# Kernel optimization log

Measured on AMD Instinct MI355X. Metric: run time of the kernel, lower is better.

The kernel has to match this reference:

```python
import jax, jax.numpy as jnp
import numpy as np

N_HEAD = 16
D_HEAD = 64
D_MODEL = 1024
N_ROLL = 3
SCALE = 1.0 / (D_HEAD ** 0.5)
EPS = 1e-5


def mul_roll_repeat(x, n_roll):
    # concat of x * roll(x, i) over i=1..n_roll along last dim
    return jnp.concatenate([x * jnp.roll(x, i, axis=-1) for i in range(1, n_roll + 1)], axis=-1)


def dpfp(x):
    # DPFP feature map: [relu(x), relu(-x)] then roll-multiply-repeat
    x2 = jnp.concatenate([jax.nn.relu(x), jax.nn.relu(-x)], axis=-1)
    return mul_roll_repeat(x2, N_ROLL)


def layer_norm(x, gamma, beta):
    mu = jnp.mean(x, axis=-1, keepdims=True)
    var = jnp.var(x, axis=-1, keepdims=True)
    return (x - mu) * jax.lax.rsqrt(var + 1e-5) * gamma + beta


def setup_inputs() -> dict:
    key = jax.random.key(0)
    ks = jax.random.split(key, 4)
    S, B = 2048, 2
    h = jax.random.normal(ks[0], (S, B, D_MODEL), dtype=jnp.float32)
    Wq = jax.random.normal(ks[1], (D_MODEL, N_HEAD * D_HEAD), dtype=jnp.float32) * 0.02
    Wkv = jax.random.normal(ks[2], (D_MODEL, 2 * N_HEAD * D_HEAD), dtype=jnp.float32) * 0.02
    Wo = jax.random.normal(ks[3], (N_HEAD * D_HEAD, D_MODEL), dtype=jnp.float32) * 0.02
    ln_gamma = jnp.ones((D_MODEL,), dtype=jnp.float32)
    ln_beta = jnp.zeros((D_MODEL,), dtype=jnp.float32)
    return {"h": h, "Wq": Wq, "Wkv": Wkv, "Wo": Wo, "ln_gamma": ln_gamma, "ln_beta": ln_beta}


def reference(h, Wq, Wkv, Wo, ln_gamma, ln_beta):
    # h: [S, B, D_MODEL]; mems=None, attn_mask=None, post-LN, eval (no dropout)
    S, B, _ = h.shape
    q = (h @ Wq).reshape(S, B, N_HEAD, D_HEAD)
    kv = h @ Wkv
    k, v = jnp.split(kv, 2, axis=-1)
    k = k.reshape(S, B, N_HEAD, D_HEAD)
    v = v.reshape(S, B, N_HEAD, D_HEAD)

    pq = dpfp(q)  # [S, B, N, F], F = 2*D_HEAD*N_ROLL = 384
    pk = dpfp(k)

    # Linear-attention form: identical math to the original quadratic
    # einsum('ibnd,jbnd->ijbn') * scale, summed over j for the denominator,
    # since there is no mask and dropatt=0. Avoids the O(S^2) score tensor.
    kv_agg = jnp.einsum('jbnf,jbnd->bnfd', pk, v)          # [B, N, F, D]
    z = pk.sum(axis=0)                                      # [B, N, F]
    num = jnp.einsum('ibnf,bnfd->ibnd', pq, kv_agg) * SCALE  # [S, B, N, D]
    den = jnp.einsum('ibnf,bnf->ibn', pq, z) * SCALE + EPS   # [S, B, N]
    attn_vec = (num / den[..., None]).reshape(S, B, N_HEAD * D_HEAD)

    attn_out = attn_vec @ Wo
    return layer_norm(h + attn_out, ln_gamma, ln_beta)
```

## Files before the change

### kernel.cpp

```cpp
#include <hip/hip_runtime.h>
#include <math.h>

#define NH 16
#define DM 1024
#define FEAT 384
#define SB 4096
#define SEQ 2048

static constexpr float SCALE = 0.125f;
static constexpr float EPS = 1e-5f;

typedef __attribute__((ext_vector_type(8))) _Float16 half8;
typedef __attribute__((ext_vector_type(4))) _Float16 half4;
typedef __attribute__((ext_vector_type(4))) float f32x4;

#define AS1 __attribute__((address_space(1)))
#define AS3 __attribute__((address_space(3)))

#define IDX(r, o) ((((r) << 6)) + ((((o) ^ ((r) & 7))) << 3))

__global__ __launch_bounds__(256) void prep_kernel(const float* __restrict__ h,
                                                   const float* __restrict__ Wq,
                                                   const float* __restrict__ Wkv,
                                                   const float* __restrict__ Wo,
                                                   _Float16* __restrict__ h_h,
                                                   _Float16* __restrict__ WqkvT,
                                                   _Float16* __restrict__ WoT) {
    __shared__ _Float16 tile[32][33];
    int bid = blockIdx.x, t = threadIdx.x;
    if (bid < 4096) {
        int i = bid * 256 + t;
        const float4 v = ((const float4*)h)[i];
        half4 o = {(_Float16)v.x, (_Float16)v.y, (_Float16)v.z, (_Float16)v.w};
        ((half4*)h_h)[i] = o;
        return;
    }
    const float* src;
    _Float16* dst;
    int N, col0, n0, k0;
    if (bid < 7168) {
        int b2 = bid - 4096;
        n0 = (b2 % 96) * 32; k0 = (b2 / 96) * 32;
        if (n0 < 1024) { src = Wq; N = 1024; col0 = n0; }
        else           { src = Wkv; N = 2048; col0 = n0 - 1024; }
        dst = WqkvT;
    } else {
        int b3 = bid - 7168;
        n0 = (b3 & 31) * 32; k0 = (b3 >> 5) * 32;
        src = Wo; N = 1024; col0 = n0; dst = WoT;
    }
    int tx = t & 31, ty = t >> 5;
    #pragma unroll
    for (int i = 0; i < 4; ++i)
        tile[ty + i * 8][tx] = (_Float16)src[(size_t)(k0 + ty + i * 8) * N + col0 + tx];
    __syncthreads();
    #pragma unroll
    for (int i = 0; i < 4; ++i)
        dst[(size_t)(n0 + ty + i * 8) * 1024 + k0 + tx] = tile[tx][ty + i * 8];
}

template <int MH>
__device__ __forceinline__ void mfma_all(f32x4 (&acc)[8][3], half8 (&a)[4][2],
                                         half8 (&bv)[3][2]) {
    #pragma unroll
    for (int mf = 0; mf < 4; ++mf)
        #pragma unroll
        for (int nf = 0; nf < 3; ++nf)
            #pragma unroll
            for (int ks = 0; ks < 2; ++ks)
                acc[MH * 4 + mf][nf] = __builtin_amdgcn_mfma_f32_16x16x32_f16(
                    a[mf][ks], bv[nf][ks], acc[MH * 4 + mf][nf], 0, 0, 0);
}

__global__ __launch_bounds__(512) void gemm_f16_8ph(const _Float16* __restrict__ A,
                                                    const _Float16* __restrict__ BT,
                                                    _Float16* __restrict__ C,
                                                    int M, int N, int K) {
    __shared__ _Float16 smem[57344];
    const int t = threadIdx.x;
    const int w = t >> 6, l = t & 63;
    const int wr = w >> 2, wc = w & 3;
    const int NT = K >> 6;
    const int NU = K >> 4;

    int nwg = gridDim.x;
    int cpx = nwg >> 3;
    int bid = blockIdx.x;
    int swz = (bid & 7) * cpx + (bid >> 3);
    int ntile = N / 192;
    int row0 = (swz / ntile) << 8;
    int col0 = (swz % ntile) * 192;

    f32x4 acc[8][3];
    #pragma unroll
    for (int m = 0; m < 8; ++m)
        #pragma unroll
        for (int n = 0; n < 3; ++n)
            acc[m][n] = (f32x4){0.f, 0.f, 0.f, 0.f};

    const int lr = l >> 3;
    const int lc8 = ((l & 7) ^ lr) * 8;

    auto STAGE = [&](int s) {
        if (s >= NU) return;
        int tau = s >> 2, u = s & 3;
        int kk = tau << 6;
        int bufo = (tau & 1) * 28672;
        if (u == 0) {
            #pragma unroll
            for (int i = 0; i < 2; ++i) {
                int chunk = w * 2 + i;
                const _Float16* src = BT + (size_t)(col0 + chunk * 8 + lr) * K + kk + lc8;
                __builtin_amdgcn_global_load_lds((const AS1 void*)src,
                    (AS3 void*)(smem + bufo + 16384 + chunk * 512), 16, 0, 0);
            }
        } else if (u == 1) {
            const _Float16* src = BT + (size_t)(col0 + 128 + w * 8 + lr) * K + kk + lc8;
            __builtin_amdgcn_global_load_lds((const AS1 void*)src,
                (AS3 void*)(smem + bufo + 24576 + w * 512), 16, 0, 0);
        } else {
            int rbase = (u == 3) ? 128 : 0;
            int lbase = (u == 3) ? 8192 : 0;
            #pragma unroll
            for (int i = 0; i < 2; ++i) {
                int chunk = w * 2 + i;
                const _Float16* src = A + (size_t)(row0 + rbase + chunk * 8 + lr) * K + kk + lc8;
                __builtin_amdgcn_global_load_lds((const AS1 void*)src,
                    (AS3 void*)(smem + bufo + lbase + chunk * 512), 16, 0, 0);
            }
        }
    };

    half8 a[4][2], bv[3][2];
    auto LDA = [&](int mh, int bufo) {
        #pragma unroll
        for (int mf = 0; mf < 4; ++mf) {
            int r = wr * 128 + (mh * 4 + mf) * 16 + (l & 15);
            #pragma unroll
            for (int ks = 0; ks < 2; ++ks) {
                int c16 = (ks * 4 + (l >> 4)) ^ (r & 7);
                a[mf][ks] = *(const half8*)&smem[bufo + r * 64 + c16 * 8];
            }
        }
    };
    auto LDB = [&](int bufo) {
        #pragma unroll
        for (int nf = 0; nf < 3; ++nf) {
            int r = wc * 48 + nf * 16 + (l & 15);
            #pragma unroll
            for (int ks = 0; ks < 2; ++ks) {
                int c16 = (ks * 4 + (l >> 4)) ^ (r & 7);
                bv[nf][ks] = *(const half8*)&smem[bufo + 16384 + r * 64 + c16 * 8];
            }
        }
    };

    STAGE(0); STAGE(1);
    STAGE(2); STAGE(3);
    STAGE(4); STAGE(5);
    asm volatile("s_waitcnt vmcnt(3)" ::: "memory");
    __builtin_amdgcn_s_barrier();

    #pragma unroll 1
    for (int ti = 0; ti < NT; ++ti) {
        const int bufo = (ti & 1) * 28672;
        const int sb = (ti + 1) << 2;
        LDA(0, bufo); LDB(bufo);
        STAGE(sb + 2); STAGE(sb + 3);
        __builtin_amdgcn_sched_barrier(0);
        __builtin_amdgcn_s_barrier();
        asm volatile("s_waitcnt lgkmcnt(0)" ::: "memory");
        __builtin_amdgcn_sched_barrier(0);
        __builtin_amdgcn_s_setprio(1);
        mfma_all<0>(acc, a, bv);
        __builtin_amdgcn_s_setprio(0);
        __builtin_amdgcn_sched_barrier(0);
        __builtin_amdgcn_s_barrier();
        LDA(1, bufo);
        STAGE(sb + 4); STAGE(sb + 5);
        __builtin_amdgcn_sched_barrier(0);
        __builtin_amdgcn_s_barrier();
        asm volatile("s_waitcnt lgkmcnt(0)" ::: "memory");
        __builtin_amdgcn_sched_barrier(0);
        __builtin_amdgcn_s_setprio(1);
        mfma_all<1>(acc, a, bv);
        __builtin_amdgcn_s_setprio(0);
        __builtin_amdgcn_sched_barrier(0);
        if (ti < NT - 2) asm volatile("s_waitcnt vmcnt(3)" ::: "memory");
        else             asm volatile("s_waitcnt vmcnt(0)" ::: "memory");
        __builtin_amdgcn_s_barrier();
    }

    int ocol = l & 15, orow4 = (l >> 4) * 4;
    #pragma unroll
    for (int mf = 0; mf < 8; ++mf)
        #pragma unroll
        for (int nf = 0; nf < 3; ++nf) {
            size_t base = (size_t)(row0 + wr * 128 + mf * 16 + orow4) * N
                        + col0 + wc * 48 + nf * 16 + ocol;
            #pragma unroll
            for (int j = 0; j < 4; ++j)
                C[base + (size_t)j * N] = (_Float16)acc[mf][nf][j];
        }
}

__global__ __launch_bounds__(256) void gemm_f16(const _Float16* __restrict__ A,
                                                const _Float16* __restrict__ BT,
                                                _Float16* __restrict__ C,
                                                int M, int N, int K) {
    __shared__ _Float16 Asb[128 * 32];
    __shared__ _Float16 Bsb[128 * 32];
    int t = threadIdx.x;
    int w = t >> 6, l = t & 63;
    int wr = w >> 1, wc = w & 1;
    int row0 = blockIdx.y * 128, col0 = blockIdx.x * 128;

    f32x4 acc[4][4];
    #pragma unroll
    for (int m = 0; m < 4; ++m)
        #pragma unroll
        for (int n = 0; n < 4; ++n)
            acc[m][n] = (f32x4){0.f, 0.f, 0.f, 0.f};

    int srow = l >> 2;
    int scol = (l & 3) * 8;

    for (int k0 = 0; k0 < K; k0 += 32) {
        #pragma unroll
        for (int i = 0; i < 2; ++i) {
            int chunk = w * 2 + i;
            const _Float16* asrc =
                A + (size_t)(row0 + chunk * 16 + srow) * K + k0 + scol;
            __builtin_amdgcn_global_load_lds((const AS1 void*)asrc,
                                             (AS3 void*)(Asb + chunk * 512), 16, 0, 0);
            const _Float16* bsrc =
                BT + (size_t)(col0 + chunk * 16 + srow) * K + k0 + scol;
            __builtin_amdgcn_global_load_lds((const AS1 void*)bsrc,
                                             (AS3 void*)(Bsb + chunk * 512), 16, 0, 0);
        }
        __syncthreads();
        int rsel = l & 15, csel = (l >> 4) * 8;
        half8 a[4], b[4];
        #pragma unroll
        for (int m = 0; m < 4; ++m)
            a[m] = *(const half8*)&Asb[(wr * 64 + m * 16 + rsel) * 32 + csel];
        #pragma unroll
        for (int n = 0; n < 4; ++n)
            b[n] = *(const half8*)&Bsb[(wc * 64 + n * 16 + rsel) * 32 + csel];
        #pragma unroll
        for (int m = 0; m < 4; ++m)
            #pragma unroll
            for (int n = 0; n < 4; ++n)
                acc[m][n] = __builtin_amdgcn_mfma_f32_16x16x32_f16(a[m], b[n], acc[m][n], 0, 0, 0);
        __syncthreads();
    }

    int ocol = l & 15, orow = (l >> 4) * 4;
    #pragma unroll
    for (int m = 0; m < 4; ++m)
        #pragma unroll
        for (int n = 0; n < 4; ++n) {
            size_t base = (size_t)(row0 + wr * 64 + m * 16 + orow) * N
                        + col0 + wc * 64 + n * 16 + ocol;
            #pragma unroll
            for (int j = 0; j < 4; ++j)
                C[base + (size_t)j * N] = (_Float16)acc[m][n][j];
        }
}

__global__ __launch_bounds__(512) void kvagg_fused(const _Float16* __restrict__ qkv,
                                                   float* __restrict__ kvp,
                                                   float* __restrict__ zp) {
    __shared__ _Float16 x2s[128 * 64];
    __shared__ _Float16 vTs[64 * 64];
    __shared__ _Float16 pkTs[384 * 64];
    const int t = threadIdx.x;
    const int w = t >> 6, l = t & 63;
    const int bn = blockIdx.x;
    const int jseg = blockIdx.y;
    const int b = bn >> 4, nh = bn & 15;

    f32x4 acc[4][3];
    #pragma unroll
    for (int mf = 0; mf < 4; ++mf)
        #pragma unroll
        for (int nf = 0; nf < 3; ++nf)
            acc[mf][nf] = (f32x4){0.f, 0.f, 0.f, 0.f};
    float zacc[3] = {0.f, 0.f, 0.f};

    const int sc = t & 63;
    const int so = t >> 6;

    #pragma unroll 1
    for (int ch = 0; ch < 4; ++ch) {
        int j0 = jseg * 256 + ch * 64;
        _Float16 kx[8], vx[8];
        #pragma unroll
        for (int e = 0; e < 8; ++e) {
            size_t rb = (size_t)((j0 + so * 8 + e) * 2 + b) * 3072 + nh * 64 + sc;
            kx[e] = qkv[rb + 1024];
            vx[e] = qkv[rb + 2048];
        }
        half8 xlo, xhi, vv;
        #pragma unroll
        for (int e = 0; e < 8; ++e) {
            float kf = (float)kx[e];
            xlo[e] = (_Float16)fmaxf(kf, 0.f);
            xhi[e] = (_Float16)fmaxf(-kf, 0.f);
            vv[e] = vx[e];
        }
        if (ch) __syncthreads();
        *(half8*)&x2s[IDX(sc, so)] = xlo;
        *(half8*)&x2s[IDX(sc + 64, so)] = xhi;
        *(half8*)&vTs[IDX(sc, so)] = vv;
        __syncthreads();
        {
            const int o = t & 7;
            const int fb = t >> 3;
            #pragma unroll
            for (int it = 0; it < 6; ++it) {
                int f = it * 64 + fb;
                int fm = f & 127;
                int r = (f >> 7) + 1;
                int fm2 = (fm - r) & 127;
                half8 pa = *(const half8*)&x2s[IDX(fm, o)];
                half8 pb = *(const half8*)&x2s[IDX(fm2, o)];
                *(half8*)&pkTs[IDX(f, o)] = pa * pb;
            }
        }
        __syncthreads();
        #pragma unroll
        for (int ks = 0; ks < 2; ++ks) {
            half8 a[4], bq[3];
            int oo = ks * 4 + (l >> 4);
            #pragma unroll
            for (int mf = 0; mf < 4; ++mf) {
                int dr = mf * 16 + (l & 15);
                a[mf] = *(const half8*)&vTs[IDX(dr, oo)];
            }
            #pragma unroll
            for (int nf = 0; nf < 3; ++nf) {
                int fr = w * 48 + nf * 16 + (l & 15);
                bq[nf] = *(const half8*)&pkTs[IDX(fr, oo)];
                #pragma unroll
                for (int e = 0; e < 8; ++e) zacc[nf] += (float)bq[nf][e];
            }
            #pragma unroll
            for (int mf = 0; mf < 4; ++mf)
                #pragma unroll
                for (int nf = 0; nf < 3; ++nf)
                    acc[mf][nf] = __builtin_amdgcn_mfma_f32_16x16x32_f16(
                        a[mf], bq[nf], acc[mf][nf], 0, 0, 0);
        }
    }

    #pragma unroll
    for (int nf = 0; nf < 3; ++nf) {
        float v = zacc[nf];
        v += __shfl_xor(v, 16, 64);
        v += __shfl_xor(v, 32, 64);
        if (l < 16)
            zp[(size_t)(jseg * 32 + bn) * FEAT + w * 48 + nf * 16 + l] = v;
    }
    float* outp = kvp + (size_t)(jseg * 32 + bn) * 64 * FEAT;
    int orow = (l >> 4) * 4, ocol = l & 15;
    #pragma unroll
    for (int mf = 0; mf < 4; ++mf)
        #pragma unroll
        for (int nf = 0; nf < 3; ++nf) {
            int fcol = w * 48 + nf * 16 + ocol;
            #pragma unroll
            for (int j = 0; j < 4; ++j)
                outp[(size_t)(mf * 16 + orow + j) * FEAT + fcol] = acc[mf][nf][j];
        }
}

__global__ __launch_bounds__(256) void reduceA(const float* __restrict__ kvp,
                                               const float* __restrict__ zp,
                                               _Float16* __restrict__ kvaggT,
                                               float* __restrict__ z) {
    const int NKV = 32 * 64 * FEAT;
    int idx = blockIdx.x * 256 + threadIdx.x;
    if (idx < NKV) {
        float s = 0.f;
        #pragma unroll
        for (int c = 0; c < 8; ++c) s += kvp[(size_t)c * NKV + idx];
        kvaggT[idx] = (_Float16)s;
    } else if (idx < NKV + 32 * FEAT) {
        int e = idx - NKV;
        float s = 0.f;
        #pragma unroll
        for (int c = 0; c < 8; ++c) s += zp[c * 32 * FEAT + e];
        z[e] = s;
    }
}

template <int F0>
__device__ __forceinline__ void pq_half(const float (&qr)[64], _Float16* prow) {
    #pragma unroll
    for (int g8 = 0; g8 < 24; ++g8) {
        half8 o;
        #pragma unroll
        for (int e = 0; e < 8; ++e) {
            const int f = F0 + g8 * 8 + e;
            const int fm = f & 127;
            const int r = (f >> 7) + 1;
            const int fm2 = (fm - r) & 127;
            float a = (fm < 64) ? fmaxf(qr[fm], 0.f) : fmaxf(-qr[fm - 64], 0.f);
            float bb = (fm2 < 64) ? fmaxf(qr[fm2], 0.f) : fmaxf(-qr[fm2 - 64], 0.f);
            o[e] = (_Float16)(a * bb);
        }
        *(half8*)&prow[F0 + g8 * 8] = o;
    }
}

#define PQ_STR 392
__global__ __launch_bounds__(256) void attn_fused(const _Float16* __restrict__ qkv,
                                                  const _Float16* __restrict__ kvaggT,
                                                  const float* __restrict__ z,
                                                  _Float16* __restrict__ av) {
    __shared__ _Float16 pq_lds[128 * PQ_STR];
    __shared__ _Float16 B_lds[64 * PQ_STR];
    __shared__ float z_lds[FEAT];
    __shared__ float den_lds[128];
    int t = threadIdx.x;
    int w = t >> 6, l = t & 63;
    int iblk = blockIdx.x;
    int bn = blockIdx.y;
    int b = bn >> 4, nh = bn & 15;

    {
        const _Float16* Bg = kvaggT + (size_t)bn * 64 * FEAT;
        #pragma unroll
        for (int s = 0; s < 12; ++s) {
            int idx8 = t + 256 * s;
            half8 vv = *(const half8*)&Bg[idx8 * 8];
            int row = idx8 / 48, col8 = idx8 - row * 48;
            *(half8*)&B_lds[row * PQ_STR + col8 * 8] = vv;
        }
    }
    for (int e = t; e < FEAT; e += 256) z_lds[e] = z[(size_t)bn * FEAT + e];

    {
        int il = t & 127;
        int ig = iblk * 128 + il;
        const _Float16* qrow = qkv + ((size_t)ig * 2 + b) * 3072 + nh * 64;
        float qr[64];
        #pragma unroll
        for (int e2 = 0; e2 < 8; ++e2) {
            half8 vv = *(const half8*)&qrow[e2 * 8];
            #pragma unroll
            for (int e = 0; e < 8; ++e) qr[e2 * 8 + e] = (float)vv[e];
        }
        _Float16* prow = &pq_lds[il * PQ_STR];
        if (t < 128) pq_half<0>(qr, prow);
        else         pq_half<192>(qr, prow);
    }
    __syncthreads();

    f32x4 acc[2][4];
    #pragma unroll
    for (int m = 0; m < 2; ++m)
        #pragma unroll
        for (int n = 0; n < 4; ++n)
            acc[m][n] = (f32x4){0.f, 0.f, 0.f, 0.f};
    float denacc[2] = {0.f, 0.f};
    int rsel = l & 15, csel = (l >> 4) * 8;

    #pragma unroll
    for (int k0 = 0; k0 < FEAT; k0 += 32) {
        half8 a[2], bfr[4];
        #pragma unroll
        for (int m = 0; m < 2; ++m)
            a[m] = *(const half8*)&pq_lds[(w * 32 + m * 16 + rsel) * PQ_STR + k0 + csel];
        #pragma unroll
        for (int n = 0; n < 4; ++n)
            bfr[n] = *(const half8*)&B_lds[(n * 16 + rsel) * PQ_STR + k0 + csel];
        #pragma unroll
        for (int m = 0; m < 2; ++m)
            #pragma unroll
            for (int e = 0; e < 8; ++e)
                denacc[m] += (float)a[m][e] * z_lds[k0 + csel + e];
        #pragma unroll
        for (int m = 0; m < 2; ++m)
            #pragma unroll
            for (int n = 0; n < 4; ++n)
                acc[m][n] = __builtin_amdgcn_mfma_f32_16x16x32_f16(a[m], bfr[n], acc[m][n], 0, 0, 0);
    }

    #pragma unroll
    for (int m = 0; m < 2; ++m) {
        float v = denacc[m];
        v += __shfl_xor(v, 16, 64);
        v += __shfl_xor(v, 32, 64);
        if (l < 16) den_lds[w * 32 + m * 16 + l] = v;
    }
    __syncthreads();

    int orow = (l >> 4) * 4, ocol = l & 15;
    #pragma unroll
    for (int m = 0; m < 2; ++m)
        #pragma unroll
        for (int n = 0; n < 4; ++n)
            #pragma unroll
            for (int j = 0; j < 4; ++j) {
                int row = w * 32 + m * 16 + orow + j;
                float den = den_lds[row] * SCALE + EPS;
                float val = acc[m][n][j] * SCALE / den;
                int i = iblk * 128 + row;
                av[((size_t)i * 2 + b) * 1024 + nh * 64 + n * 16 + ocol] = (_Float16)val;
            }
}

__global__ __launch_bounds__(256) void ln_kernel(const float* __restrict__ h,
                                                 const _Float16* __restrict__ attn_out,
                                                 const float* __restrict__ gamma,
                                                 const float* __restrict__ beta,
                                                 float* __restrict__ out) {
    int r = blockIdx.x;
    int t = threadIdx.x;
    const float4 hv = ((const float4*)(h + (size_t)r * 1024))[t];
    const half4 a4 = ((const half4*)(attn_out + (size_t)r * 1024))[t];
    float x[4] = {hv.x + (float)a4[0], hv.y + (float)a4[1],
                  hv.z + (float)a4[2], hv.w + (float)a4[3]};
    float sum = x[0] + x[1] + x[2] + x[3];
    float sq = x[0]*x[0] + x[1]*x[1] + x[2]*x[2] + x[3]*x[3];
    #pragma unroll
    for (int off = 32; off >= 1; off >>= 1) {
        sum += __shfl_xor(sum, off, 64);
        sq += __shfl_xor(sq, off, 64);
    }
    __shared__ float ssum[4], ssq[4];
    int wl = t >> 6, lane = t & 63;
    if (lane == 0) { ssum[wl] = sum; ssq[wl] = sq; }
    __syncthreads();
    sum = ssum[0] + ssum[1] + ssum[2] + ssum[3];
    sq = ssq[0] + ssq[1] + ssq[2] + ssq[3];
    float mu = sum * (1.f / 1024.f);
    float var = sq * (1.f / 1024.f) - mu * mu;
    float rs = rsqrtf(var + 1e-5f);
    const float4 g4 = ((const float4*)gamma)[t];
    const float4 b4 = ((const float4*)beta)[t];
    float4 o;
    o.x = (x[0] - mu) * rs * g4.x + b4.x;
    o.y = (x[1] - mu) * rs * g4.y + b4.y;
    o.z = (x[2] - mu) * rs * g4.z + b4.z;
    o.w = (x[3] - mu) * rs * g4.w + b4.w;
    ((float4*)(out + (size_t)r * 1024))[t] = o;
}

extern "C" void kernel_launch(void* const* d_in, const int* in_sizes, int n_in,
                              void* d_out, int out_size, void* d_ws, size_t ws_size,
                              hipStream_t stream) {
    const float* h     = (const float*)d_in[0];
    const float* Wq    = (const float*)d_in[1];
    const float* Wkv   = (const float*)d_in[2];
    const float* Wo    = (const float*)d_in[3];
    const float* gamma = (const float*)d_in[4];
    const float* beta  = (const float*)d_in[5];
    float* out = (float*)d_out;
    _Float16* u = (_Float16*)d_ws;

    _Float16* h_h    = u;
    _Float16* WqkvT  = u + 4194304;
    _Float16* WoT    = u + 7340032;
    _Float16* qkv    = u + 8388608;
    float*    kvp    = (float*)(u + 20971520);
    float*    zp     = (float*)(u + 33554432);
    _Float16* kvaggT = u + 33751040;
    float*    z      = (float*)(u + 34537472);
    _Float16* av         = h_h;
    _Float16* attn_out_h = qkv;

    dim3 blk(256);
    prep_kernel<<<dim3(8192), blk, 0, stream>>>(h, Wq, Wkv, Wo, h_h, WqkvT, WoT);
    gemm_f16_8ph<<<dim3(256), dim3(512), 0, stream>>>(h_h, WqkvT, qkv, SB, 3072, DM);
    kvagg_fused<<<dim3(32, 8), dim3(512), 0, stream>>>(qkv, kvp, zp);
    reduceA<<<dim3(3120), blk, 0, stream>>>(kvp, zp, kvaggT, z);
    attn_fused<<<dim3(16, 32), blk, 0, stream>>>(qkv, kvaggT, z, av);
    gemm_f16<<<dim3(8, 32), blk, 0, stream>>>(av, WoT, attn_out_h, SB, 1024, DM);
    ln_kernel<<<dim3(SB), blk, 0, stream>>>(h, attn_out_h, gamma, beta, out);
}
```

Baseline: 111.4 us.

## Build DPFP query features in registers from a compact relu buffer

Instead of materializing the 384-wide DPFP query features for 128 rows in shared memory, the attention kernel now stores only the 128-wide relu split (with a wraparound pad) for 64 rows. Each lane then forms its A fragments in registers by multiplying rolled elements. The B tile drops its padded stride for an XOR swizzle, and the grid doubles to 64 rows per block, which cuts LDS usage and should raise occupancy. The trade-off is fewer MFMAs per block and extra register pressure from holding 16 half8 values plus 12 fragments. Feature products are now computed in fp16 rather than fp32, which slightly changes rounding.

```diff
diff --git a/kernel.cpp b/kernel.cpp
--- a/kernel.cpp
+++ b/kernel.cpp
@@ -395,121 +395,112 @@
     }
 }
 
-template <int F0>
-__device__ __forceinline__ void pq_half(const float (&qr)[64], _Float16* prow) {
-    #pragma unroll
-    for (int g8 = 0; g8 < 24; ++g8) {
-        half8 o;
-        #pragma unroll
-        for (int e = 0; e < 8; ++e) {
-            const int f = F0 + g8 * 8 + e;
-            const int fm = f & 127;
-            const int r = (f >> 7) + 1;
-            const int fm2 = (fm - r) & 127;
-            float a = (fm < 64) ? fmaxf(qr[fm], 0.f) : fmaxf(-qr[fm - 64], 0.f);
-            float bb = (fm2 < 64) ? fmaxf(qr[fm2], 0.f) : fmaxf(-qr[fm2 - 64], 0.f);
-            o[e] = (_Float16)(a * bb);
-        }
-        *(half8*)&prow[F0 + g8 * 8] = o;
-    }
-}
-
-#define PQ_STR 392
+#define X2STR 152
 __global__ __launch_bounds__(256) void attn_fused(const _Float16* __restrict__ qkv,
                                                   const _Float16* __restrict__ kvaggT,
                                                   const float* __restrict__ z,
                                                   _Float16* __restrict__ av) {
-    __shared__ _Float16 pq_lds[128 * PQ_STR];
-    __shared__ _Float16 B_lds[64 * PQ_STR];
+    __shared__ _Float16 x2e[64 * X2STR];
+    __shared__ _Float16 B_lds[64 * FEAT];
     __shared__ float z_lds[FEAT];
-    __shared__ float den_lds[128];
-    int t = threadIdx.x;
-    int w = t >> 6, l = t & 63;
-    int iblk = blockIdx.x;
-    int bn = blockIdx.y;
-    int b = bn >> 4, nh = bn & 15;
+    __shared__ float den_lds[64];
+    const int t = threadIdx.x;
+    const int w = t >> 6, l = t & 63;
+    const int iblk = blockIdx.x;
+    const int bn = blockIdx.y;
+    const int b = bn >> 4, nh = bn & 15;
 
     {
         const _Float16* Bg = kvaggT + (size_t)bn * 64 * FEAT;
         #pragma unroll
         for (int s = 0; s < 12; ++s) {
             int idx8 = t + 256 * s;
-            half8 vv = *(const half8*)&Bg[idx8 * 8];
-            int row = idx8 / 48, col8 = idx8 - row * 48;
-            *(half8*)&B_lds[row * PQ_STR + col8 * 8] = vv;
+            int row = idx8 / 48, c16 = idx8 - row * 48;
+            half8 vv = *(const half8*)&Bg[row * FEAT + c16 * 8];
+            *(half8*)&B_lds[row * FEAT + ((c16 ^ (row & 7)) << 3)] = vv;
         }
     }
     for (int e = t; e < FEAT; e += 256) z_lds[e] = z[(size_t)bn * FEAT + e];
 
     {
-        int il = t & 127;
-        int ig = iblk * 128 + il;
-        const _Float16* qrow = qkv + ((size_t)ig * 2 + b) * 3072 + nh * 64;
-        float qr[64];
-        #pragma unroll
-        for (int e2 = 0; e2 < 8; ++e2) {
-            half8 vv = *(const half8*)&qrow[e2 * 8];
-            #pragma unroll
-            for (int e = 0; e < 8; ++e) qr[e2 * 8 + e] = (float)vv[e];
-        }
-        _Float16* prow = &pq_lds[il * PQ_STR];
-        if (t < 128) pq_half<0>(qr, prow);
-        else         pq_half<192>(qr, prow);
+        int row = t >> 2, c0 = (t & 3) * 16;
+        const _Float16* qrow = qkv + (size_t)((iblk * 64 + row) * 2 + b) * 3072 + nh * 64;
+        half8 q0 = *(const half8*)&qrow[c0];
+        half8 q1 = *(const half8*)&qrow[c0 + 8];
+        half8 lo0, lo1, hi0, hi1;
+        #pragma unroll
+        for (int e = 0; e < 8; ++e) {
+            float f0 = (float)q0[e], f1 = (float)q1[e];
+            lo0[e] = (_Float16)fmaxf(f0, 0.f);
+            lo1[e] = (_Float16)fmaxf(f1, 0.f);
+            hi0[e] = (_Float16)fmaxf(-f0, 0.f);
+            hi1[e] = (_Float16)fmaxf(-f1, 0.f);
+        }
+        _Float16* xr = &x2e[row * X2STR];
+        *(half8*)&xr[c0] = lo0;
+        *(half8*)&xr[c0 + 8] = lo1;
+        *(half8*)&xr[64 + c0] = hi0;
+        *(half8*)&xr[64 + c0 + 8] = hi1;
+        if (c0 == 0) { *(half8*)&xr[128] = lo0; *(half8*)&xr[136] = lo1; }
+        if (c0 == 16) { *(half8*)&xr[144] = lo0; }
     }
     __syncthreads();
 
-    f32x4 acc[2][4];
-    #pragma unroll
-    for (int m = 0; m < 2; ++m)
-        #pragma unroll
-        for (int n = 0; n < 4; ++n)
-            acc[m][n] = (f32x4){0.f, 0.f, 0.f, 0.f};
-    float denacc[2] = {0.f, 0.f};
-    int rsel = l & 15, csel = (l >> 4) * 8;
-
-    #pragma unroll
-    for (int k0 = 0; k0 < FEAT; k0 += 32) {
-        half8 a[2], bfr[4];
-        #pragma unroll
-        for (int m = 0; m < 2; ++m)
-            a[m] = *(const half8*)&pq_lds[(w * 32 + m * 16 + rsel) * PQ_STR + k0 + csel];
-        #pragma unroll
-        for (int n = 0; n < 4; ++n)
-            bfr[n] = *(const half8*)&B_lds[(n * 16 + rsel) * PQ_STR + k0 + csel];
-        #pragma unroll
-        for (int m = 0; m < 2; ++m)
-            #pragma unroll
-            for (int e = 0; e < 8; ++e)
-                denacc[m] += (float)a[m][e] * z_lds[k0 + csel + e];
-        #pragma unroll
-        for (int m = 0; m < 2; ++m)
-            #pragma unroll
-            for (int n = 0; n < 4; ++n)
-                acc[m][n] = __builtin_amdgcn_mfma_f32_16x16x32_f16(a[m], bfr[n], acc[m][n], 0, 0, 0);
-    }
-
-    #pragma unroll
-    for (int m = 0; m < 2; ++m) {
-        float v = denacc[m];
-        v += __shfl_xor(v, 16, 64);
-        v += __shfl_xor(v, 32, 64);
-        if (l < 16) den_lds[w * 32 + m * 16 + l] = v;
-    }
+    const int rloc16 = l & 15;
+    const int csel = (l >> 4) * 8;
+    const int lrow = w * 16 + rloc16;
+    half8 y8[16];
+    {
+        const _Float16* xr = &x2e[lrow * X2STR + csel];
+        #pragma unroll
+        for (int j = 0; j < 16; ++j)
+            y8[j] = *(const half8*)&xr[j * 8];
+    }
+    half8 afr[12];
+    #pragma unroll
+    for (int ks = 0; ks < 12; ++ks) {
+        const int r = (ks >> 2) + 1;
+        #pragma unroll
+        for (int e = 0; e < 8; ++e) {
+            const int j1 = ((ks & 3) * 32 + e) & 127;
+            const int j2 = ((ks & 3) * 32 + e - r) & 127;
+            afr[ks][e] = y8[j1 >> 3][j1 & 7] * y8[j2 >> 3][j2 & 7];
+        }
+    }
+
+    f32x4 acc[4];
+    #pragma unroll
+    for (int n = 0; n < 4; ++n) acc[n] = (f32x4){0.f, 0.f, 0.f, 0.f};
+    float den = 0.f;
+    #pragma unroll
+    for (int ks = 0; ks < 12; ++ks) {
+        #pragma unroll
+        for (int e = 0; e < 8; ++e)
+            den += (float)afr[ks][e] * z_lds[ks * 32 + csel + e];
+        #pragma unroll
+        for (int nf = 0; nf < 4; ++nf) {
+            int row = nf * 16 + rloc16;
+            int c16 = (ks * 4 + (l >> 4)) ^ (row & 7);
+            half8 bfr = *(const half8*)&B_lds[row * FEAT + (c16 << 3)];
+            acc[nf] = __builtin_amdgcn_mfma_f32_16x16x32_f16(afr[ks], bfr, acc[nf], 0, 0, 0);
+        }
+    }
+
+    den += __shfl_xor(den, 16, 64);
+    den += __shfl_xor(den, 32, 64);
+    if (l < 16) den_lds[w * 16 + l] = den;
     __syncthreads();
 
-    int orow = (l >> 4) * 4, ocol = l & 15;
-    #pragma unroll
-    for (int m = 0; m < 2; ++m)
-        #pragma unroll
-        for (int n = 0; n < 4; ++n)
-            #pragma unroll
-            for (int j = 0; j < 4; ++j) {
-                int row = w * 32 + m * 16 + orow + j;
-                float den = den_lds[row] * SCALE + EPS;
-                float val = acc[m][n][j] * SCALE / den;
-                int i = iblk * 128 + row;
-                av[((size_t)i * 2 + b) * 1024 + nh * 64 + n * 16 + ocol] = (_Float16)val;
-            }
+    #pragma unroll
+    for (int nf = 0; nf < 4; ++nf)
+        #pragma unroll
+        for (int j = 0; j < 4; ++j) {
+            int rl = w * 16 + (l >> 4) * 4 + j;
+            float dv = den_lds[rl] * SCALE + EPS;
+            float val = acc[nf][j] * SCALE / dv;
+            int i = iblk * 64 + rl;
+            av[((size_t)i * 2 + b) * 1024 + nh * 64 + nf * 16 + (l & 15)] = (_Float16)val;
+        }
 }
 
 __global__ __launch_bounds__(256) void ln_kernel(const float* __restrict__ h,
@@ -577,7 +568,7 @@
     gemm_f16_8ph<<<dim3(256), dim3(512), 0, stream>>>(h_h, WqkvT, qkv, SB, 3072, DM);
     kvagg_fused<<<dim3(32, 8), dim3(512), 0, stream>>>(qkv, kvp, zp);
     reduceA<<<dim3(3120), blk, 0, stream>>>(kvp, zp, kvaggT, z);
-    attn_fused<<<dim3(16, 32), blk, 0, stream>>>(qkv, kvaggT, z, av);
+    attn_fused<<<dim3(32, 32), blk, 0, stream>>>(qkv, kvaggT, z, av);
     gemm_f16<<<dim3(8, 32), blk, 0, stream>>>(av, WoT, attn_out_h, SB, 1024, DM);
     ln_kernel<<<dim3(SB), blk, 0, stream>>>(h, attn_out_h, gamma, beta, out);
 }
```

Result: faster. 108.4 us (-2.7%).
